# Kernel optimization log

Measured on AMD Instinct MI355X. Metric: run time of the kernel, lower is better.

## Reference

```python
import jax, jax.numpy as jnp
import numpy as np

B, S, H, NH, NKV, HD, E, I = 1, 2048, 1024, 16, 8, 64, 8, 2048
TOPK = 2
EPS = 1e-6
THETA = 1e6


def setup_inputs() -> dict:
    key = jax.random.key(0)
    ks = jax.random.split(key, 12)
    init = lambda k, shp: jax.random.normal(k, shp, jnp.float32) * 0.02
    hidden_states = jax.random.normal(ks[0], (B, S, H), jnp.float32)
    attention_mask = jnp.ones((B, S), jnp.float32)
    position_ids = jnp.broadcast_to(jnp.arange(S, dtype=jnp.int32), (B, S))
    inv_freq = 1.0 / (THETA ** (jnp.arange(0, HD, 2, dtype=jnp.float32) / HD))
    freqs = jnp.outer(jnp.arange(S, dtype=jnp.float32), inv_freq)  # [S, HD/2]
    emb = jnp.concatenate([freqs, freqs], axis=-1)                  # [S, HD]
    return dict(
        hidden_states=hidden_states,
        attention_mask=attention_mask,
        position_ids=position_ids,
        sin=jnp.sin(emb), cos=jnp.cos(emb),
        wq=init(ks[1], (H, NH * HD)),
        wk=init(ks[2], (H, NKV * HD)),
        wv=init(ks[3], (H, NKV * HD)),
        wo=init(ks[4], (NH * HD, H)),
        ln1=jnp.ones((H,), jnp.float32),
        ln2=jnp.ones((H,), jnp.float32),
        gate_w=init(ks[5], (H, E)),
        w1=init(ks[6], (E, H, I)),
        w3=init(ks[7], (E, H, I)),
        w2=init(ks[8], (E, I, H)),
    )


def _rms_norm(x, w):
    return x * jax.lax.rsqrt(jnp.mean(jnp.square(x), -1, keepdims=True) + EPS) * w


def _rotate_half(x):
    h = x.shape[-1] // 2
    return jnp.concatenate([-x[..., h:], x[..., :h]], axis=-1)


def reference(hidden_states, attention_mask, position_ids, sin, cos,
              wq, wk, wv, wo, ln1, ln2, gate_w, w1, w3, w2):
    x = hidden_states
    # ---- self-attention block ----
    h = _rms_norm(x, ln1)
    q = (h @ wq).reshape(B, S, NH, HD).transpose(0, 2, 1, 3)    # [B,NH,S,HD]
    k = (h @ wk).reshape(B, S, NKV, HD).transpose(0, 2, 1, 3)   # [B,NKV,S,HD]
    v = (h @ wv).reshape(B, S, NKV, HD).transpose(0, 2, 1, 3)
    sb = sin[position_ids][:, None]  # [B,1,S,HD]
    cb = cos[position_ids][:, None]
    q = q * cb + _rotate_half(q) * sb
    k = k * cb + _rotate_half(k) * sb
    rep = NH // NKV
    k = jnp.repeat(k, rep, axis=1)  # GQA repeat -> [B,NH,S,HD]
    v = jnp.repeat(v, rep, axis=1)
    causal = jnp.tril(jnp.ones((S, S), bool))
    mask = causal[None, None] & (attention_mask[:, None, None, :] > 0)
    bias = jnp.where(mask, 0.0, jnp.finfo(jnp.float32).min)
    scale = 1.0 / jnp.sqrt(jnp.float32(HD))
    scores = jnp.einsum('bhqd,bhkd->bhqk', q, k) * scale + bias
    attn = jax.nn.softmax(scores, axis=-1)
    o = jnp.einsum('bhqk,bhkd->bhqd', attn, v)
    o = o.transpose(0, 2, 1, 3).reshape(B, S, NH * HD) @ wo
    x = x + o
    # ---- sparse MoE block (top-2 of E experts, SiLU-gated MLP) ----
    t = _rms_norm(x, ln2).reshape(B * S, H)
    router_logits = t @ gate_w                         # [T,E]
    probs = jax.nn.softmax(router_logits, axis=-1)
    top_w, top_i = jax.lax.top_k(probs, TOPK)          # [T,2]
    top_w = top_w / jnp.sum(top_w, axis=-1, keepdims=True)
    full_w = jnp.sum(jax.nn.one_hot(top_i, E, dtype=t.dtype) * top_w[..., None], axis=1)  # [T,E]
    moe_out = jnp.zeros_like(t)
    for e in range(E):  # fixed small expert count
        ge = jax.nn.silu(t @ w1[e]) * (t @ w3[e])      # [T,I]
        moe_out = moe_out + full_w[:, e:e + 1] * (ge @ w2[e])
    x = x + moe_out.reshape(B, S, H)
    return x
```

## Files before the change

### kernel.cpp

```cpp
#include <hip/hip_runtime.h>

#define S 2048
#define H 1024
#define NH 16
#define NKV 8
#define HD 64
#define NE 8
#define ID 2048

typedef short bf16x8 __attribute__((ext_vector_type(8)));
typedef short bf16x4 __attribute__((ext_vector_type(4)));
typedef float f32x4 __attribute__((ext_vector_type(4)));

__device__ __forceinline__ unsigned short f2bf(float f) {
  unsigned u = __builtin_bit_cast(unsigned, f);
  u += 0x7FFFu + ((u >> 16) & 1u);
  return (unsigned short)(u >> 16);
}
__device__ __forceinline__ float bf2f(unsigned short h) {
  unsigned u = ((unsigned)h) << 16;
  return __builtin_bit_cast(float, u);
}
__device__ __forceinline__ unsigned cvtpk(float a, float b) {
  unsigned r;
  asm("v_cvt_pk_bf16_f32 %0, %1, %2" : "=v"(r) : "v"(a), "v"(b));
  return r;
}

typedef const __attribute__((address_space(1))) unsigned int gas_u32;
typedef __attribute__((address_space(3))) unsigned int las_u32;
__device__ __forceinline__ void gload16(const unsigned short* g, unsigned short* l) {
  __builtin_amdgcn_global_load_lds((gas_u32*)g, (las_u32*)l, 16, 0, 0);
}

template <bool LO>
__device__ __forceinline__ void tconv_tile128(const float* __restrict__ src,
                                              unsigned short* __restrict__ hi,
                                              unsigned short* __restrict__ lo, int K, int N,
                                              int nt, int kt, float (*tile)[65]) {
  int tid = threadIdx.x;
  int wv = tid >> 6, ln = tid & 63;
  const float* sb = src + (size_t)(kt * 128) * N + nt * 64 + ln;
#pragma unroll 8
  for (int rr = 0; rr < 32; rr++) {
    int r = rr * 4 + wv;
    tile[r][ln] = sb[(size_t)r * N];
  }
  __syncthreads();
  int seg = tid & 15;
  int rq = tid >> 4;
#pragma unroll
  for (int it = 0; it < 4; it++) {
    int row = it * 16 + rq;
    int cs = seg * 8;
    size_t dbase = (size_t)(nt * 64 + row) * K + kt * 128 + cs;
    unsigned short th[8], tl[8];
#pragma unroll
    for (int i = 0; i < 8; i++) {
      float vv = tile[cs + i][row];
      unsigned short h_ = f2bf(vv);
      th[i] = h_;
      if (LO) tl[i] = f2bf(vv - bf2f(h_));
    }
    *(bf16x8*)(hi + dbase) = *(bf16x8*)&th[0];
    if (LO) *(bf16x8*)(lo + dbase) = *(bf16x8*)&tl[0];
  }
}

__global__ __launch_bounds__(256) void prep_kernel(
    const float* __restrict__ x, const float* __restrict__ ln1,
    unsigned short* __restrict__ h_hi, unsigned short* __restrict__ h_lo,
    const float* __restrict__ wq, const float* __restrict__ wk, const float* __restrict__ wv,
    const float* __restrict__ wo, unsigned short* __restrict__ wqkvT_hi,
    unsigned short* __restrict__ wqkvT_lo, unsigned short* __restrict__ woT_hi,
    unsigned short* __restrict__ woT_lo) {
  __shared__ float tile[128][65];
  __shared__ float part[4];
  int u = blockIdx.x, grp = u / 19, slot = u % 19;
  int tid = threadIdx.x;
  if (slot < 16) {
    int row = grp * 16 + slot;
    const float* xr = x + (size_t)row * H;
    float v[4];
    float ss = 0.f;
#pragma unroll
    for (int i = 0; i < 4; i++) {
      v[i] = xr[tid + i * 256];
      ss += v[i] * v[i];
    }
#pragma unroll
    for (int off = 1; off < 64; off <<= 1) ss += __shfl_xor(ss, off);
    if ((tid & 63) == 0) part[tid >> 6] = ss;
    __syncthreads();
    float tot = part[0] + part[1] + part[2] + part[3];
    float r = rsqrtf(tot * (1.f / H) + 1e-6f);
#pragma unroll
    for (int i = 0; i < 4; i++) {
      int c = tid + i * 256;
      float vv = v[i] * r * ln1[c];
      size_t o = (size_t)row * H + c;
      unsigned short h_ = f2bf(vv);
      h_hi[o] = h_;
      h_lo[o] = f2bf(vv - bf2f(h_));
    }
  } else {
    int local = grp * 3 + (slot - 16);
    const float* src;
    unsigned short *hi, *lo;
    int N, l2;
    if (local < 128) {
      src = wq; hi = wqkvT_hi; lo = wqkvT_lo; N = 1024; l2 = local;
    } else if (local < 192) {
      src = wk; hi = wqkvT_hi + (size_t)1024 * 1024; lo = wqkvT_lo + (size_t)1024 * 1024; N = 512; l2 = local - 128;
    } else if (local < 256) {
      src = wv; hi = wqkvT_hi + (size_t)1536 * 1024; lo = wqkvT_lo + (size_t)1536 * 1024; N = 512; l2 = local - 192;
    } else {
      src = wo; hi = woT_hi; lo = woT_lo; N = 1024; l2 = local - 256;
    }
    int ntc = N >> 6;
    int nt = l2 % ntc, kt = l2 / ntc;
    tconv_tile128<true>(src, hi, lo, 1024, N, nt, kt, tile);
  }
}

__global__ __launch_bounds__(256) void rv_kernel(
    const float* __restrict__ qkv, const float* __restrict__ sinb,
    const float* __restrict__ cosb, const int* __restrict__ pos,
    unsigned short* __restrict__ qhi, unsigned short* __restrict__ qlo,
    unsigned short* __restrict__ khi, unsigned short* __restrict__ klo,
    unsigned short* __restrict__ vThi, unsigned short* __restrict__ vTlo) {
  __shared__ float tile[64][65];
  int u = blockIdx.x, grp = u / 25, slot = u % 25;
  int tid = threadIdx.x;
  if (slot == 0) {
    int st = grp & 31, hk = grp >> 5;
    int r = tid >> 2, seg = (tid & 3) * 16;
    const float* src = qkv + (size_t)(st * 64 + r) * 2048 + 1536 + hk * HD + seg;
#pragma unroll
    for (int i = 0; i < 16; i += 4) {
      float4 a = *(const float4*)(src + i);
      tile[r][seg + i] = a.x;
      tile[r][seg + i + 1] = a.y;
      tile[r][seg + i + 2] = a.z;
      tile[r][seg + i + 3] = a.w;
    }
    __syncthreads();
    int d = tid >> 2, ss = (tid & 3) * 16;
    unsigned short th[16], tl[16];
#pragma unroll
    for (int i = 0; i < 16; i++) {
      float vv = tile[ss + i][d];
      unsigned short h_ = f2bf(vv);
      th[i] = h_;
      tl[i] = f2bf(vv - bf2f(h_));
    }
    size_t dst = ((size_t)hk * HD + d) * S + st * 64 + ss;
    *(bf16x8*)(vThi + dst) = *(bf16x8*)&th[0];
    *(bf16x8*)(vThi + dst + 8) = *(bf16x8*)&th[8];
    *(bf16x8*)(vTlo + dst) = *(bf16x8*)&tl[0];
    *(bf16x8*)(vTlo + dst + 8) = *(bf16x8*)&tl[8];
  } else {
    int i = (grp * 24 + slot - 1) * 256 + tid;
    int d = i & 31;
    int s = (i >> 5) & 2047;
    int hh = i >> 16;
    int p = pos[s];
    float c0 = cosb[p * HD + d], c1 = cosb[p * HD + d + 32];
    float s0 = sinb[p * HD + d], s1 = sinb[p * HD + d + 32];
    const float* srcb = qkv + (size_t)s * 2048;
    if (hh < NH) {
      float x0 = srcb[hh * HD + d], x1 = srcb[hh * HD + d + 32];
      float r0 = (x0 * c0 - x1 * s0) * 0.125f;
      float r1 = (x1 * c1 + x0 * s1) * 0.125f;
      size_t o = ((size_t)hh * S + s) * HD + d;
      unsigned short h0 = f2bf(r0), h1 = f2bf(r1);
      qhi[o] = h0;
      qlo[o] = f2bf(r0 - bf2f(h0));
      qhi[o + 32] = h1;
      qlo[o + 32] = f2bf(r1 - bf2f(h1));
    } else {
      int hk = hh - NH;
      float x0 = srcb[1024 + hk * HD + d], x1 = srcb[1024 + hk * HD + d + 32];
      float r0 = x0 * c0 - x1 * s0;
      float r1 = x1 * c1 + x0 * s1;
      size_t o = ((size_t)hk * S + s) * HD + d;
      unsigned short h0 = f2bf(r0), h1 = f2bf(r1);
      khi[o] = h0;
      klo[o] = f2bf(r0 - bf2f(h0));
      khi[o + 32] = h1;
      klo[o + 32] = f2bf(r1 - bf2f(h1));
    }
  }
}

__global__ __launch_bounds__(256, 4) void gemm1_w13_kernel(
    const unsigned short* __restrict__ oh, const unsigned short* __restrict__ ol,
    const unsigned short* __restrict__ woh, const unsigned short* __restrict__ wol,
    float* __restrict__ x2, float* __restrict__ out, const float* __restrict__ resid,
    const float* __restrict__ w1, const float* __restrict__ w3,
    unsigned short* __restrict__ w1T, unsigned short* __restrict__ w3T) {
  __shared__ __align__(16) char smem[33280];
  int u = blockIdx.x, grp = u / 9, slot = u % 9;
  int tid = threadIdx.x;
  if (slot != 0) {
    int t = grp * 8 + slot - 1;
    int b = t >> 8, rem = t & 255, kt = rem >> 5, nt = rem & 31;
    const float* src = (b < 8) ? w1 + (size_t)b * 1024 * 2048 : w3 + (size_t)(b - 8) * 1024 * 2048;
    unsigned short* hi = (b < 8) ? w1T + (size_t)b * 2048 * 1024 : w3T + (size_t)(b - 8) * 2048 * 1024;
    tconv_tile128<false>(src, hi, nullptr, 1024, 2048, nt, kt, (float(*)[65])smem);
    return;
  }
  int g = grp;
  int bx = g & 15, by = g >> 4;
  unsigned short* tAh = (unsigned short*)smem;
  unsigned short* tAl = tAh + 4096;
  unsigned short* tBh = tAl + 4096;
  unsigned short* tBl = tBh + 4096;
  int n0 = bx * 64, m0 = by * 64;
  int w = tid >> 6, lane = tid & 63;
  int lr = lane & 15, gq = lane >> 4;
  int rloc = lane >> 3, slotg = (lane & 7) ^ rloc;
  int wm = w >> 1, wn = w & 1;
  unsigned aOff[2], bOff[2];
#pragma unroll
  for (int cc = 0; cc < 2; cc++) {
    int rr = (w * 2 + cc) * 8 + rloc;
    aOff[cc] = (unsigned)((m0 + rr) * 1024 + slotg * 8);
    bOff[cc] = (unsigned)((n0 + rr) * 1024 + slotg * 8);
  }
  f32x4 acc[2][2];
#pragma unroll
  for (int i = 0; i < 2; i++)
#pragma unroll
    for (int j = 0; j < 2; j++) acc[i][j] = f32x4{0.f, 0.f, 0.f, 0.f};
  for (int k0 = 0; k0 < 1024; k0 += 64) {
    __syncthreads();
#pragma unroll
    for (int cc = 0; cc < 2; cc++) {
      int cb = (w * 2 + cc) * 512;
      gload16(oh + aOff[cc] + k0, &tAh[cb]);
      gload16(ol + aOff[cc] + k0, &tAl[cb]);
      gload16(woh + bOff[cc] + k0, &tBh[cb]);
      gload16(wol + bOff[cc] + k0, &tBl[cb]);
    }
    __syncthreads();
    bf16x8 fah[2][2], fal[2][2];
#pragma unroll
    for (int i = 0; i < 2; i++) {
      int ar = wm * 32 + i * 16 + lr;
#pragma unroll
      for (int kk = 0; kk < 2; kk++) {
        int off = ar * 64 + (((kk * 4 + gq) ^ (ar & 7)) * 8);
        fah[i][kk] = *(const bf16x8*)&tAh[off];
        fal[i][kk] = *(const bf16x8*)&tAl[off];
      }
    }
#pragma unroll
    for (int j = 0; j < 2; j++) {
      int br = wn * 32 + j * 16 + lr;
      bf16x8 fbh[2], fbl[2];
#pragma unroll
      for (int kk = 0; kk < 2; kk++) {
        int off = br * 64 + (((kk * 4 + gq) ^ (br & 7)) * 8);
        fbh[kk] = *(const bf16x8*)&tBh[off];
        fbl[kk] = *(const bf16x8*)&tBl[off];
      }
#pragma unroll
      for (int i = 0; i < 2; i++) {
#pragma unroll
        for (int kk = 0; kk < 2; kk++) {
          acc[i][j] = __builtin_amdgcn_mfma_f32_16x16x32_bf16(fah[i][kk], fbh[kk], acc[i][j], 0, 0, 0);
          acc[i][j] = __builtin_amdgcn_mfma_f32_16x16x32_bf16(fah[i][kk], fbl[kk], acc[i][j], 0, 0, 0);
          acc[i][j] = __builtin_amdgcn_mfma_f32_16x16x32_bf16(fal[i][kk], fbh[kk], acc[i][j], 0, 0, 0);
        }
      }
    }
  }
#pragma unroll
  for (int i = 0; i < 2; i++)
#pragma unroll
    for (int j = 0; j < 2; j++)
#pragma unroll
      for (int r = 0; r < 4; r++) {
        int grow = wm * 32 + i * 16 + gq * 4 + r;
        int gcol = n0 + wn * 32 + j * 16 + lr;
        float o = acc[i][j][r] + resid[(size_t)(m0 + grow) * 1024 + gcol];
        x2[(size_t)(m0 + grow) * 1024 + gcol] = o;
        out[(size_t)(m0 + grow) * 1024 + gcol] = o;
      }
}

__global__ __launch_bounds__(256) void rmsnorm_router_kernel(
    const float* __restrict__ x, const float* __restrict__ wgt,
    const float* __restrict__ gw, unsigned short* __restrict__ ohi,
    int* __restrict__ selE, float* __restrict__ selW) {
  int row = blockIdx.x;
  const float* xr = x + (size_t)row * H;
  int tid = threadIdx.x;
  float v[4];
  float ss = 0.f;
#pragma unroll
  for (int i = 0; i < 4; i++) {
    v[i] = xr[tid + i * 256];
    ss += v[i] * v[i];
  }
#pragma unroll
  for (int off = 1; off < 64; off <<= 1) ss += __shfl_xor(ss, off);
  __shared__ float part[4];
  __shared__ float red[4][NE];
  if ((tid & 63) == 0) part[tid >> 6] = ss;
  __syncthreads();
  float tot = part[0] + part[1] + part[2] + part[3];
  float r = rsqrtf(tot * (1.f / H) + 1e-6f);
  float acc[NE];
#pragma unroll
  for (int e = 0; e < NE; e++) acc[e] = 0.f;
#pragma unroll
  for (int i = 0; i < 4; i++) {
    int c = tid + i * 256;
    float vv = v[i] * r * wgt[c];
    ohi[(size_t)row * H + c] = f2bf(vv);
    const float4* gp = (const float4*)(gw + (size_t)c * NE);
    float4 g0 = gp[0], g1 = gp[1];
    acc[0] += vv * g0.x;
    acc[1] += vv * g0.y;
    acc[2] += vv * g0.z;
    acc[3] += vv * g0.w;
    acc[4] += vv * g1.x;
    acc[5] += vv * g1.y;
    acc[6] += vv * g1.z;
    acc[7] += vv * g1.w;
  }
#pragma unroll
  for (int off = 1; off < 64; off <<= 1) {
#pragma unroll
    for (int e = 0; e < NE; e++) acc[e] += __shfl_xor(acc[e], off);
  }
  if ((tid & 63) == 0) {
#pragma unroll
    for (int e = 0; e < NE; e++) red[tid >> 6][e] = acc[e];
  }
  __syncthreads();
  if (tid == 0) {
    float lg[NE];
#pragma unroll
    for (int e = 0; e < NE; e++) lg[e] = red[0][e] + red[1][e] + red[2][e] + red[3][e];
    int e1 = 0;
#pragma unroll
    for (int e = 1; e < NE; e++)
      if (lg[e] > lg[e1]) e1 = e;
    int e2 = -1;
#pragma unroll
    for (int e = 0; e < NE; e++)
      if (e != e1 && (e2 < 0 || lg[e] > lg[e2])) e2 = e;
    float w1v = 1.f / (1.f + __expf(lg[e2] - lg[e1]));
    selE[row] = e1 | (e2 << 8);
    selW[row * 2] = w1v;
    selW[row * 2 + 1] = 1.f - w1v;
  }
}

__global__ __launch_bounds__(256) void assign_kernel(const int* __restrict__ selE,
                                                     int* __restrict__ cnt,
                                                     int* __restrict__ offs,
                                                     int* __restrict__ tmap,
                                                     int* __restrict__ idxb,
                                                     int* __restrict__ tokslot) {
  int tid = threadIdx.x;
  __shared__ int sc[256][NE];
  int pack[8];
  int hist[NE];
#pragma unroll
  for (int e = 0; e < NE; e++) hist[e] = 0;
#pragma unroll
  for (int i = 0; i < 8; i++) {
    pack[i] = selE[tid * 8 + i];
    hist[pack[i] & 255]++;
    hist[(pack[i] >> 8) & 255]++;
  }
#pragma unroll
  for (int e = 0; e < NE; e++) sc[tid][e] = hist[e];
  __syncthreads();
  for (int off = 1; off < 256; off <<= 1) {
    int add[NE];
    bool has = tid >= off;
    if (has) {
#pragma unroll
      for (int e = 0; e < NE; e++) add[e] = sc[tid - off][e];
    }
    __syncthreads();
    if (has) {
#pragma unroll
      for (int e = 0; e < NE; e++) sc[tid][e] += add[e];
    }
    __syncthreads();
  }
  int offsL[NE];
  {
    int a = 0;
#pragma unroll
    for (int e = 0; e < NE; e++) {
      offsL[e] = a;
      a += sc[255][e];
    }
  }
  if (tid == 0) {
    int t = 0;
    for (int e = 0; e < NE; e++) {
      int totE = sc[255][e];
      offs[e] = offsL[e];
      cnt[e] = totE;
      int nt = (totE + 127) >> 7;
      for (int i = 0; i < nt; i++) tmap[t++] = (e << 16) | i;
    }
    offs[NE] = offsL[NE - 1] + sc[255][NE - 1];
    tmap[63] = t;
  }
  int run[NE];
#pragma unroll
  for (int e = 0; e < NE; e++) run[e] = sc[tid][e] - hist[e];
#pragma unroll
  for (int i = 0; i < 8; i++) {
    int tok = tid * 8 + i;
    int e1 = pack[i] & 255, e2 = (pack[i] >> 8) & 255;
    int p1 = run[e1]++;
    idxb[e1 * S + p1] = tok;
    int p2 = run[e2]++;
    idxb[e2 * S + p2] = tok;
    tokslot[tok * 2] = offsL[e1] + p1;
    tokslot[tok * 2 + 1] = offsL[e2] + p2;
  }
}

__global__ __launch_bounds__(256) void moe_gather_kernel(const float* __restrict__ moeP,
                                                         const int* __restrict__ tokslot,
                                                         const float* __restrict__ selW,
                                                         float* __restrict__ out) {
  int tok = blockIdx.x;
  int c = threadIdx.x * 4;
  int s0 = tokslot[tok * 2], s1 = tokslot[tok * 2 + 1];
  float w0 = selW[tok * 2], w1 = selW[tok * 2 + 1];
  const float* P0 = moeP;
  const float* P1 = moeP + (size_t)4096 * 1024;
  float4 a0 = *(const float4*)(P0 + (size_t)s0 * 1024 + c);
  float4 b0 = *(const float4*)(P1 + (size_t)s0 * 1024 + c);
  float4 a1 = *(const float4*)(P0 + (size_t)s1 * 1024 + c);
  float4 b1 = *(const float4*)(P1 + (size_t)s1 * 1024 + c);
  float* op = out + (size_t)tok * 1024 + c;
  float4 o = *(float4*)op;
  o.x += w0 * (a0.x + b0.x) + w1 * (a1.x + b1.x);
  o.y += w0 * (a0.y + b0.y) + w1 * (a1.y + b1.y);
  o.z += w0 * (a0.z + b0.z) + w1 * (a1.z + b1.z);
  o.w += w0 * (a0.w + b0.w) + w1 * (a1.w + b1.w);
  *(float4*)op = o;
}

__global__ __launch_bounds__(256, 4) void tconv_w2_kernel(const float* __restrict__ w2,
                                                          unsigned short* __restrict__ w2T) {
  __shared__ float tile[128][65];
  int b = blockIdx.z;
  tconv_tile128<false>(w2 + (size_t)b * 2048 * 1024, w2T + (size_t)b * 1024 * 2048, nullptr, 2048,
                       1024, blockIdx.x, blockIdx.y, tile);
}

template <int MODE>
__global__ __launch_bounds__(256, 4) void gemm_kernel(
    const unsigned short* __restrict__ Ah, const unsigned short* __restrict__ Al,
    const unsigned short* __restrict__ Bh, const unsigned short* __restrict__ Bl,
    float* __restrict__ C, unsigned short* __restrict__ Gout,
    const int* __restrict__ idx, const int* __restrict__ cnt, const int* __restrict__ offs,
    const int* __restrict__ tmap, int N, int K) {
  constexpr int BM = (MODE <= 1) ? 64 : 128;
  constexpr int NI = BM / 32;
  int n0 = blockIdx.x * 64, m0, e = 0;
  int ce = 0, gbase = 0;
  if (MODE >= 2) {
    int ntiles = tmap[63];
    if ((int)blockIdx.y >= ntiles) return;
    int packed = tmap[blockIdx.y];
    e = packed >> 16;
    m0 = (packed & 0xffff) * 128;
    ce = cnt[e];
    gbase = offs[e];
  } else {
    m0 = blockIdx.y * BM;
  }
  const unsigned short* bhp = Bh;
  const unsigned short* blp = Bl;
  if (MODE == 2) {
    bhp += (size_t)e * 2048 * 1024;
    blp += (size_t)e * 2048 * 1024;
  }
  if (MODE == 3) bhp += (size_t)e * 1024 * 2048;

  __shared__ __align__(16) unsigned short tAh[BM * 64];
  __shared__ __align__(16) unsigned short tAl[MODE <= 1 ? BM * 64 : 8];
  __shared__ __align__(16) unsigned short tBh[64 * 64];
  __shared__ __align__(16) unsigned short tBl[MODE <= 2 ? 64 * 64 : 8];

  int tid = threadIdx.x, w = tid >> 6, lane = tid & 63;
  int lr = lane & 15, g = lane >> 4;
  int rloc = lane >> 3, slotg = (lane & 7) ^ rloc;
  int wm = w >> 1, wn = w & 1;

  unsigned aOff[NI], bOff[2];
#pragma unroll
  for (int cc = 0; cc < NI; cc++) {
    int rr = (w * NI + cc) * 8 + rloc;
    if (MODE == 2) {
      int gr = m0 + rr;
      if (gr > ce - 1) gr = ce - 1;
      int tok = idx[e * S + gr];
      aOff[cc] = (unsigned)(tok * K + slotg * 8);
    } else if (MODE == 3) {
      int gr = gbase + m0 + rr;
      if (gr > 4095) gr = 4095;
      aOff[cc] = (unsigned)(gr * K + slotg * 8);
    } else {
      aOff[cc] = (unsigned)((m0 + rr) * K + slotg * 8);
    }
  }
#pragma unroll
  for (int cc = 0; cc < 2; cc++) {
    int rr = (w * 2 + cc) * 8 + rloc;
    bOff[cc] = (unsigned)((n0 + rr) * K + slotg * 8);
  }

  f32x4 acc[NI][2], acc2[NI][2];
#pragma unroll
  for (int i = 0; i < NI; i++)
#pragma unroll
    for (int j = 0; j < 2; j++) {
      acc[i][j] = f32x4{0.f, 0.f, 0.f, 0.f};
      if (MODE == 2) acc2[i][j] = f32x4{0.f, 0.f, 0.f, 0.f};
    }

  int kbeg = 0, kend = K;
  if (MODE == 3) {
    kbeg = (int)blockIdx.z * (K >> 1);
    kend = kbeg + (K >> 1);
  }
  for (int k0 = kbeg; k0 < kend; k0 += 64) {
    __syncthreads();
#pragma unroll
    for (int cc = 0; cc < NI; cc++) {
      int cb = (w * NI + cc) * 512;
      gload16(Ah + aOff[cc] + k0, &tAh[cb]);
      if (MODE <= 1) gload16(Al + aOff[cc] + k0, &tAl[cb]);
    }
#pragma unroll
    for (int cc = 0; cc < 2; cc++) {
      int cb = (w * 2 + cc) * 512;
      gload16(bhp + bOff[cc] + k0, &tBh[cb]);
      if (MODE <= 2) gload16(blp + bOff[cc] + k0, &tBl[cb]);
    }
    __syncthreads();
    bf16x8 fah[NI][2], fal[NI][2];
#pragma unroll
    for (int i = 0; i < NI; i++) {
      int ar = wm * (BM / 2) + i * 16 + lr;
#pragma unroll
      for (int kk = 0; kk < 2; kk++) {
        int off = ar * 64 + (((kk * 4 + g) ^ (ar & 7)) * 8);
        fah[i][kk] = *(const bf16x8*)&tAh[off];
        if (MODE <= 1) fal[i][kk] = *(const bf16x8*)&tAl[off];
      }
    }
#pragma unroll
    for (int j = 0; j < 2; j++) {
      int br = wn * 32 + j * 16 + lr;
      bf16x8 fbh[2], fbl[2];
#pragma unroll
      for (int kk = 0; kk < 2; kk++) {
        int off = br * 64 + (((kk * 4 + g) ^ (br & 7)) * 8);
        fbh[kk] = *(const bf16x8*)&tBh[off];
        if (MODE <= 2) fbl[kk] = *(const bf16x8*)&tBl[off];
      }
#pragma unroll
      for (int i = 0; i < NI; i++) {
#pragma unroll
        for (int kk = 0; kk < 2; kk++) {
          acc[i][j] = __builtin_amdgcn_mfma_f32_16x16x32_bf16(fah[i][kk], fbh[kk], acc[i][j], 0, 0, 0);
          if (MODE <= 1) {
            acc[i][j] = __builtin_amdgcn_mfma_f32_16x16x32_bf16(fah[i][kk], fbl[kk], acc[i][j], 0, 0, 0);
            acc[i][j] = __builtin_amdgcn_mfma_f32_16x16x32_bf16(fal[i][kk], fbh[kk], acc[i][j], 0, 0, 0);
          }
          if (MODE == 2)
            acc2[i][j] = __builtin_amdgcn_mfma_f32_16x16x32_bf16(fah[i][kk], fbl[kk], acc2[i][j], 0, 0, 0);
        }
      }
    }
  }
#pragma unroll
  for (int i = 0; i < NI; i++)
#pragma unroll
    for (int j = 0; j < 2; j++)
#pragma unroll
      for (int r = 0; r < 4; r++) {
        int grow = wm * (BM / 2) + i * 16 + g * 4 + r;
        int gcol = n0 + wn * 32 + j * 16 + lr;
        float v = acc[i][j][r];
        if (MODE == 0) {
          C[(size_t)(m0 + grow) * N + gcol] = v;
        } else if (MODE == 2) {
          if (m0 + grow < ce) {
            float g3 = acc2[i][j][r];
            float sg = v / (1.f + __expf(-v));
            Gout[(size_t)(gbase + m0 + grow) * 2048 + gcol] = f2bf(sg * g3);
          }
        } else if (MODE == 3) {
          if (m0 + grow < ce) {
            C[(size_t)blockIdx.z * 4096 * 1024 + (size_t)(gbase + m0 + grow) * 1024 + gcol] = v;
          }
        }
      }
}

#define FSWZ(row, byteoff) ((byteoff) ^ (((row) & 7) << 4))

__global__ __launch_bounds__(256, 4) void flash_kernel(
    const unsigned short* __restrict__ qhi, const unsigned short* __restrict__ qlo,
    const unsigned short* __restrict__ khip, const unsigned short* __restrict__ klop,
    const unsigned short* __restrict__ vthip, const unsigned short* __restrict__ vtlop,
    const float* __restrict__ amask, float* __restrict__ po, float* __restrict__ pm,
    float* __restrict__ pl) {
  int u = blockIdx.x;
  int r_ = u >> 8, base = u & 255;
  int qt = (base + r_ * 8) & 31;
  int head = ((base >> 5) & 7) | ((r_ & 1) << 3);
  int z = r_ >> 1;
  int tid = threadIdx.x;
  int w = tid >> 6, lane = tid & 63;
  int lr = lane & 15, g = lane >> 4;
  int rloc = lane >> 3, slotg = (lane & 7) ^ rloc;

  __shared__ __align__(16) unsigned short Khi[64 * 64];
  __shared__ __align__(16) unsigned short Klo[64 * 64];
  __shared__ __align__(16) unsigned short Vhi[64 * 64];
  __shared__ __align__(16) unsigned short Vlo[64 * 64];
  __shared__ __align__(16) unsigned short Pbuf[4][16 * 64];

  int qrow = qt * 64 + w * 16 + lr;
  bf16x8 qh[2], ql[2];
  {
    const unsigned short* qb = qhi + ((size_t)head * S + qrow) * HD;
    const unsigned short* qb2 = qlo + ((size_t)head * S + qrow) * HD;
    qh[0] = *(const bf16x8*)(qb + g * 8);
    qh[1] = *(const bf16x8*)(qb + 32 + g * 8);
    ql[0] = *(const bf16x8*)(qb2 + g * 8);
    ql[1] = *(const bf16x8*)(qb2 + 32 + g * 8);
  }

  f32x4 oacc[4];
#pragma unroll
  for (int dg = 0; dg < 4; dg++) oacc[dg] = f32x4{0.f, 0.f, 0.f, 0.f};
  float m = -1e30f, l = 0.f;

  const unsigned short* kbh = khip + (size_t)(head >> 1) * S * HD;
  const unsigned short* kbl = klop + (size_t)(head >> 1) * S * HD;
  const unsigned short* vbh = vthip + (size_t)(head >> 1) * HD * S;
  const unsigned short* vbl = vtlop + (size_t)(head >> 1) * HD * S;
  char* pbase = (char*)Pbuf[w];

  int nblk = qt + 1;
  int b0 = (z * nblk) >> 1, b1 = ((z + 1) * nblk) >> 1;

  for (int kb = b0; kb < b1; kb++) {
    int kv0 = kb * 64;
    __syncthreads();
#pragma unroll
    for (int cc = 0; cc < 2; cc++) {
      int c = w * 2 + cc;
      int r = c * 8 + rloc;
      gload16(kbh + (size_t)(kv0 + r) * HD + slotg * 8, &Khi[c * 512]);
      gload16(kbl + (size_t)(kv0 + r) * HD + slotg * 8, &Klo[c * 512]);
      gload16(vbh + (size_t)r * S + kv0 + slotg * 8, &Vhi[c * 512]);
      gload16(vbl + (size_t)r * S + kv0 + slotg * 8, &Vlo[c * 512]);
    }
    unsigned long long vm = __ballot(amask[kv0 + lane] > 0.f);
    __syncthreads();

    f32x4 sacc[4];
#pragma unroll
    for (int c = 0; c < 4; c++) sacc[c] = f32x4{0.f, 0.f, 0.f, 0.f};
#pragma unroll
    for (int c = 0; c < 4; c++) {
#pragma unroll
      for (int kc = 0; kc < 2; kc++) {
        int row = c * 16 + lr;
        int bo = FSWZ(row, row * 128 + kc * 64 + g * 16);
        bf16x8 khf = *(const bf16x8*)((char*)Khi + bo);
        bf16x8 klf = *(const bf16x8*)((char*)Klo + bo);
        sacc[c] = __builtin_amdgcn_mfma_f32_16x16x32_bf16(khf, qh[kc], sacc[c], 0, 0, 0);
        sacc[c] = __builtin_amdgcn_mfma_f32_16x16x32_bf16(khf, ql[kc], sacc[c], 0, 0, 0);
        sacc[c] = __builtin_amdgcn_mfma_f32_16x16x32_bf16(klf, qh[kc], sacc[c], 0, 0, 0);
      }
    }
    int qloc = w * 16 + lr;
    bool diag = (kb == qt);
    bool fullvis = (vm == ~0ull) && !diag;
    float tm = -1e30f;
    if (fullvis) {
#pragma unroll
      for (int c = 0; c < 4; c++)
#pragma unroll
        for (int r = 0; r < 4; r++) tm = fmaxf(tm, sacc[c][r]);
    } else {
#pragma unroll
      for (int c = 0; c < 4; c++) {
#pragma unroll
        for (int r = 0; r < 4; r++) {
          int kvloc = c * 16 + 4 * g + r;
          bool vis = ((vm >> kvloc) & 1ull) && (!diag || kvloc <= qloc);
          float sv = vis ? sacc[c][r] : -1e30f;
          sacc[c][r] = sv;
          tm = fmaxf(tm, sv);
        }
      }
    }
    tm = fmaxf(tm, __shfl_xor(tm, 16));
    tm = fmaxf(tm, __shfl_xor(tm, 32));
    bool skip = __all(tm - m <= 8.f);
    float newm = skip ? m : fmaxf(m, tm);
    float rs = 0.f;
#pragma unroll
    for (int c = 0; c < 4; c++) {
#pragma unroll
      for (int r = 0; r < 4; r++) {
        float p = __expf(sacc[c][r] - newm);
        sacc[c][r] = p;
        rs += p;
      }
    }
    rs += __shfl_xor(rs, 16);
    rs += __shfl_xor(rs, 32);
    if (!skip) {
      float alpha = __expf(m - newm);
      m = newm;
      l = l * alpha + rs;
#pragma unroll
      for (int dg = 0; dg < 4; dg++) {
#pragma unroll
        for (int r = 0; r < 4; r++) oacc[dg][r] *= alpha;
      }
    } else {
      l += rs;
    }
    unsigned hw[4][2];
#pragma unroll
    for (int c = 0; c < 4; c++) {
      hw[c][0] = cvtpk(sacc[c][0], sacc[c][1]);
      hw[c][1] = cvtpk(sacc[c][2], sacc[c][3]);
      uint2 hv = {hw[c][0], hw[c][1]};
      *(uint2*)(pbase + FSWZ(lr, lr * 128 + (c * 16 + 4 * g) * 2)) = hv;
    }
    bf16x8 pbh[2], pbl[2];
#pragma unroll
    for (int kc = 0; kc < 2; kc++)
      pbh[kc] = *(const bf16x8*)(pbase + FSWZ(lr, lr * 128 + kc * 64 + g * 16));
#pragma unroll
    for (int c = 0; c < 4; c++) {
      float h0 = __builtin_bit_cast(float, hw[c][0] << 16);
      float h1 = __builtin_bit_cast(float, hw[c][0] & 0xffff0000u);
      float h2 = __builtin_bit_cast(float, hw[c][1] << 16);
      float h3 = __builtin_bit_cast(float, hw[c][1] & 0xffff0000u);
      uint2 lv = {cvtpk(sacc[c][0] - h0, sacc[c][1] - h1),
                  cvtpk(sacc[c][2] - h2, sacc[c][3] - h3)};
      *(uint2*)(pbase + FSWZ(lr, lr * 128 + (c * 16 + 4 * g) * 2)) = lv;
    }
#pragma unroll
    for (int kc = 0; kc < 2; kc++)
      pbl[kc] = *(const bf16x8*)(pbase + FSWZ(lr, lr * 128 + kc * 64 + g * 16));
#pragma unroll
    for (int dg = 0; dg < 4; dg++) {
#pragma unroll
      for (int kc = 0; kc < 2; kc++) {
        int row = dg * 16 + lr;
        int bo = FSWZ(row, row * 128 + kc * 64 + g * 16);
        bf16x8 vhf = *(const bf16x8*)((char*)Vhi + bo);
        bf16x8 vlf = *(const bf16x8*)((char*)Vlo + bo);
        oacc[dg] = __builtin_amdgcn_mfma_f32_16x16x32_bf16(vhf, pbh[kc], oacc[dg], 0, 0, 0);
        oacc[dg] = __builtin_amdgcn_mfma_f32_16x16x32_bf16(vhf, pbl[kc], oacc[dg], 0, 0, 0);
        oacc[dg] = __builtin_amdgcn_mfma_f32_16x16x32_bf16(vlf, pbh[kc], oacc[dg], 0, 0, 0);
      }
    }
  }

  size_t pb = (size_t)(qt * 16 + head) * 2 + z;
  int row = w * 16 + lr;
  if (g == 0) {
    pm[pb * 64 + row] = m;
    pl[pb * 64 + row] = l;
  }
  float* pob = po + pb * 4096 + (size_t)row * 64;
#pragma unroll
  for (int dg = 0; dg < 4; dg++) {
    float4 v4 = {oacc[dg][0], oacc[dg][1], oacc[dg][2], oacc[dg][3]};
    *(float4*)(pob + dg * 16 + 4 * g) = v4;
  }
}

__global__ __launch_bounds__(256) void combine_kernel(const float* __restrict__ po,
                                                      const float* __restrict__ pm,
                                                      const float* __restrict__ pl,
                                                      unsigned short* __restrict__ ohi,
                                                      unsigned short* __restrict__ olo) {
  int qt = blockIdx.x, head = blockIdx.y;
  int r = threadIdx.x >> 2, dg = (threadIdx.x & 3) * 16;
  size_t base = (size_t)(qt * 16 + head) * 2;
  float m0v = pm[base * 64 + r], m1v = pm[(base + 1) * 64 + r];
  float l0 = pl[base * 64 + r], l1 = pl[(base + 1) * 64 + r];
  float M = fmaxf(m0v, m1v);
  float w0 = __expf(m0v - M), w1 = __expf(m1v - M);
  float inv = 1.f / (w0 * l0 + w1 * l1);
  const float* p0 = po + base * 4096 + (size_t)r * 64 + dg;
  const float* p1 = po + (base + 1) * 4096 + (size_t)r * 64 + dg;
  unsigned short th[16], tl[16];
#pragma unroll
  for (int i = 0; i < 16; i += 4) {
    float4 a = *(const float4*)(p0 + i);
    float4 b = *(const float4*)(p1 + i);
    float vv[4] = {(w0 * a.x + w1 * b.x) * inv, (w0 * a.y + w1 * b.y) * inv,
                   (w0 * a.z + w1 * b.z) * inv, (w0 * a.w + w1 * b.w) * inv};
#pragma unroll
    for (int j = 0; j < 4; j++) {
      unsigned short h_ = f2bf(vv[j]);
      th[i + j] = h_;
      tl[i + j] = f2bf(vv[j] - bf2f(h_));
    }
  }
  size_t ob = (size_t)(qt * 64 + r) * 1024 + head * 64 + dg;
  *(bf16x8*)(ohi + ob) = *(bf16x8*)&th[0];
  *(bf16x8*)(ohi + ob + 8) = *(bf16x8*)&th[8];
  *(bf16x8*)(olo + ob) = *(bf16x8*)&tl[0];
  *(bf16x8*)(olo + ob + 8) = *(bf16x8*)&tl[8];
}

extern "C" void kernel_launch(void* const* d_in, const int* in_sizes, int n_in,
                              void* d_out, int out_size, void* d_ws, size_t ws_size,
                              hipStream_t stream) {
  const float* x = (const float*)d_in[0];
  const float* amask = (const float*)d_in[1];
  const int* pos = (const int*)d_in[2];
  const float* sinb = (const float*)d_in[3];
  const float* cosb = (const float*)d_in[4];
  const float* wq = (const float*)d_in[5];
  const float* wk = (const float*)d_in[6];
  const float* wv = (const float*)d_in[7];
  const float* wo = (const float*)d_in[8];
  const float* ln1 = (const float*)d_in[9];
  const float* ln2 = (const float*)d_in[10];
  const float* gw = (const float*)d_in[11];
  const float* w1 = (const float*)d_in[12];
  const float* w3 = (const float*)d_in[13];
  const float* w2 = (const float*)d_in[14];
  float* out = (float*)d_out;

  char* ws = (char*)d_ws;
  const size_t MB = 1024 * 1024;
  float* x2 = (float*)(ws + 0 * MB);
  unsigned short* t_bf = (unsigned short*)(ws + 8 * MB);
  int* cnt = (int*)(ws + 12 * MB);
  int* offs = cnt + 16;
  int* tmap = cnt + 32;
  int* idxb = cnt + 128;
  int* selE = idxb + 16384;
  int* tokslot = selE + 2048;
  float* selW = (float*)(tokslot + 4096);
  unsigned short* o_hi = (unsigned short*)(ws + 13 * MB);
  unsigned short* o_lo = (unsigned short*)(ws + 17 * MB);
  unsigned short* G = (unsigned short*)(ws + 13 * MB);
  float* qkv = (float*)(ws + 13 * MB);
  unsigned short* w1T = (unsigned short*)(ws + 29 * MB);
  unsigned short* w3T = (unsigned short*)(ws + 61 * MB);
  unsigned short* w2T = (unsigned short*)(ws + 29 * MB);
  float* moeP = (float*)(ws + 61 * MB);
  float* po = (float*)(ws + 29 * MB);
  float* pm = (float*)(ws + 45 * MB);
  float* pl = (float*)(ws + 46 * MB);
  unsigned short* wqkvT_hi = (unsigned short*)(ws + 47 * MB);
  unsigned short* wqkvT_lo = (unsigned short*)(ws + 51 * MB);
  unsigned short* h_hi = (unsigned short*)(ws + 55 * MB);
  unsigned short* h_lo = (unsigned short*)(ws + 59 * MB);
  unsigned short* q_hi = (unsigned short*)(ws + 63 * MB);
  unsigned short* q_lo = (unsigned short*)(ws + 67 * MB);
  unsigned short* k_hi = (unsigned short*)(ws + 71 * MB);
  unsigned short* k_lo = (unsigned short*)(ws + 73 * MB);
  unsigned short* vT_hi = (unsigned short*)(ws + 75 * MB);
  unsigned short* vT_lo = (unsigned short*)(ws + 77 * MB);
  unsigned short* woT_hi = (unsigned short*)(ws + 93 * MB);
  unsigned short* woT_lo = (unsigned short*)(ws + 95 * MB);

  prep_kernel<<<2432, 256, 0, stream>>>(x, ln1, h_hi, h_lo, wq, wk, wv, wo, wqkvT_hi, wqkvT_lo,
                                        woT_hi, woT_lo);
  gemm_kernel<0><<<dim3(32, 32, 1), 256, 0, stream>>>(h_hi, h_lo, wqkvT_hi, wqkvT_lo, qkv, nullptr,
                                                      nullptr, nullptr, nullptr, nullptr, 2048,
                                                      1024);
  rv_kernel<<<6400, 256, 0, stream>>>(qkv, sinb, cosb, pos, q_hi, q_lo, k_hi, k_lo, vT_hi, vT_lo);
  flash_kernel<<<dim3(1024, 1, 1), 256, 0, stream>>>(q_hi, q_lo, k_hi, k_lo, vT_hi, vT_lo, amask,
                                                     po, pm, pl);
  combine_kernel<<<dim3(32, 16), 256, 0, stream>>>(po, pm, pl, o_hi, o_lo);
  gemm1_w13_kernel<<<4608, 256, 0, stream>>>(o_hi, o_lo, woT_hi, woT_lo, x2, out, x, w1, w3, w1T,
                                             w3T);
  rmsnorm_router_kernel<<<S, 256, 0, stream>>>(x2, ln2, gw, t_bf, selE, selW);
  assign_kernel<<<1, 256, 0, stream>>>(selE, cnt, offs, tmap, idxb, tokslot);
  gemm_kernel<2><<<dim3(32, 40, 1), 256, 0, stream>>>(t_bf, nullptr, w1T, w3T, nullptr, G, idxb,
                                                      cnt, offs, tmap, 2048, 1024);
  tconv_w2_kernel<<<dim3(16, 16, 8), 256, 0, stream>>>(w2, w2T);
  gemm_kernel<3><<<dim3(16, 40, 2), 256, 0, stream>>>(G, nullptr, w2T, nullptr, moeP, nullptr,
                                                      idxb, cnt, offs, tmap, 1024, 2048);
  moe_gather_kernel<<<S, 256, 0, stream>>>(moeP, tokslot, selW, out);
}
```

Baseline: 281.3 us.

## Fuse w2 transpose-convert into grouped w1/w3 MoE GEMM launch

Merges the expert w1/w3 gated GEMM and the w2 transpose/bf16 conversion into one kernel launch. Blocks are interleaved in groups of 13: 5 GEMM tiles and 8 transpose tiles, so the memory-bound conversion can run alongside the compute-bound GEMM. w2T moves to its own workspace region so it no longer aliases w1T. This removes a launch boundary and idle tail, at the cost of the shared-memory footprint being sized for the larger of the two roles.

```diff
diff --git a/kernel.cpp b/kernel.cpp
--- a/kernel.cpp
+++ b/kernel.cpp
@@ -290,6 +290,123 @@
       }
 }
 
+__global__ __launch_bounds__(256, 4) void gemm2_w2_kernel(
+    const unsigned short* __restrict__ Ah, const unsigned short* __restrict__ w1T,
+    const unsigned short* __restrict__ w3T, unsigned short* __restrict__ Gout,
+    const int* __restrict__ idx, const int* __restrict__ cnt, const int* __restrict__ offs,
+    const int* __restrict__ tmap, const float* __restrict__ w2,
+    unsigned short* __restrict__ w2T) {
+  __shared__ __align__(16) char smem[33280];
+  int u = blockIdx.x, grp = u / 13, slot = u % 13;
+  int tid = threadIdx.x;
+  if (slot >= 5) {
+    int t = grp * 8 + slot - 5;
+    int b = t >> 8, rem = t & 255, kt = rem >> 4, nt = rem & 15;
+    tconv_tile128<false>(w2 + (size_t)b * 2048 * 1024, w2T + (size_t)b * 1024 * 2048, nullptr,
+                         2048, 1024, nt, kt, (float(*)[65])smem);
+    return;
+  }
+  int g = grp * 5 + slot;
+  int bx = g & 31, ty = g >> 5;
+  int ntiles = tmap[63];
+  if (ty >= ntiles) return;
+  int packed = tmap[ty];
+  int e = packed >> 16;
+  int m0 = (packed & 0xffff) * 128;
+  int ce = cnt[e];
+  int gbase = offs[e];
+  const unsigned short* bhp = w1T + (size_t)e * 2048 * 1024;
+  const unsigned short* blp = w3T + (size_t)e * 2048 * 1024;
+  unsigned short* tAh = (unsigned short*)smem;
+  unsigned short* tBh = tAh + 8192;
+  unsigned short* tBl = tBh + 4096;
+  int n0 = bx * 64;
+  int w = tid >> 6, lane = tid & 63;
+  int lr = lane & 15, gq = lane >> 4;
+  int rloc = lane >> 3, slotg = (lane & 7) ^ rloc;
+  int wm = w >> 1, wn = w & 1;
+  unsigned aOff[4], bOff[2];
+#pragma unroll
+  for (int cc = 0; cc < 4; cc++) {
+    int rr = (w * 4 + cc) * 8 + rloc;
+    int gr = m0 + rr;
+    if (gr > ce - 1) gr = ce - 1;
+    int tok = idx[e * S + gr];
+    aOff[cc] = (unsigned)(tok * 1024 + slotg * 8);
+  }
+#pragma unroll
+  for (int cc = 0; cc < 2; cc++) {
+    int rr = (w * 2 + cc) * 8 + rloc;
+    bOff[cc] = (unsigned)((n0 + rr) * 1024 + slotg * 8);
+  }
+  f32x4 acc[4][2], acc2[4][2];
+#pragma unroll
+  for (int i = 0; i < 4; i++)
+#pragma unroll
+    for (int j = 0; j < 2; j++) {
+      acc[i][j] = f32x4{0.f, 0.f, 0.f, 0.f};
+      acc2[i][j] = f32x4{0.f, 0.f, 0.f, 0.f};
+    }
+  for (int k0 = 0; k0 < 1024; k0 += 64) {
+    __syncthreads();
+#pragma unroll
+    for (int cc = 0; cc < 4; cc++) {
+      gload16(Ah + aOff[cc] + k0, &tAh[(w * 4 + cc) * 512]);
+    }
+#pragma unroll
+    for (int cc = 0; cc < 2; cc++) {
+      int cb = (w * 2 + cc) * 512;
+      gload16(bhp + bOff[cc] + k0, &tBh[cb]);
+      gload16(blp + bOff[cc] + k0, &tBl[cb]);
+    }
+    __syncthreads();
+    bf16x8 fah[4][2];
+#pragma unroll
+    for (int i = 0; i < 4; i++) {
+      int ar = wm * 64 + i * 16 + lr;
+#pragma unroll
+      for (int kk = 0; kk < 2; kk++) {
+        int off = ar * 64 + (((kk * 4 + gq) ^ (ar & 7)) * 8);
+        fah[i][kk] = *(const bf16x8*)&tAh[off];
+      }
+    }
+#pragma unroll
+    for (int j = 0; j < 2; j++) {
+      int br = wn * 32 + j * 16 + lr;
+      bf16x8 fbh[2], fbl[2];
+#pragma unroll
+      for (int kk = 0; kk < 2; kk++) {
+        int off = br * 64 + (((kk * 4 + gq) ^ (br & 7)) * 8);
+        fbh[kk] = *(const bf16x8*)&tBh[off];
+        fbl[kk] = *(const bf16x8*)&tBl[off];
+      }
+#pragma unroll
+      for (int i = 0; i < 4; i++) {
+#pragma unroll
+        for (int kk = 0; kk < 2; kk++) {
+          acc[i][j] = __builtin_amdgcn_mfma_f32_16x16x32_bf16(fah[i][kk], fbh[kk], acc[i][j], 0, 0, 0);
+          acc2[i][j] = __builtin_amdgcn_mfma_f32_16x16x32_bf16(fah[i][kk], fbl[kk], acc2[i][j], 0, 0, 0);
+        }
+      }
+    }
+  }
+#pragma unroll
+  for (int i = 0; i < 4; i++)
+#pragma unroll
+    for (int j = 0; j < 2; j++)
+#pragma unroll
+      for (int r = 0; r < 4; r++) {
+        int grow = wm * 64 + i * 16 + gq * 4 + r;
+        int gcol = n0 + wn * 32 + j * 16 + lr;
+        if (m0 + grow < ce) {
+          float v = acc[i][j][r];
+          float g3 = acc2[i][j][r];
+          float sg = v / (1.f + __expf(-v));
+          Gout[(size_t)(gbase + m0 + grow) * 2048 + gcol] = f2bf(sg * g3);
+        }
+      }
+}
+
 __global__ __launch_bounds__(256) void rmsnorm_router_kernel(
     const float* __restrict__ x, const float* __restrict__ wgt,
     const float* __restrict__ gw, unsigned short* __restrict__ ohi,
@@ -455,14 +572,6 @@
   *(float4*)op = o;
 }
 
-__global__ __launch_bounds__(256, 4) void tconv_w2_kernel(const float* __restrict__ w2,
-                                                          unsigned short* __restrict__ w2T) {
-  __shared__ float tile[128][65];
-  int b = blockIdx.z;
-  tconv_tile128<false>(w2 + (size_t)b * 2048 * 1024, w2T + (size_t)b * 1024 * 2048, nullptr, 2048,
-                       1024, blockIdx.x, blockIdx.y, tile);
-}
-
 template <int MODE>
 __global__ __launch_bounds__(256, 4) void gemm_kernel(
     const unsigned short* __restrict__ Ah, const unsigned short* __restrict__ Al,
@@ -487,10 +596,6 @@
   }
   const unsigned short* bhp = Bh;
   const unsigned short* blp = Bl;
-  if (MODE == 2) {
-    bhp += (size_t)e * 2048 * 1024;
-    blp += (size_t)e * 2048 * 1024;
-  }
   if (MODE == 3) bhp += (size_t)e * 1024 * 2048;
 
   __shared__ __align__(16) unsigned short tAh[BM * 64];
@@ -507,12 +612,7 @@
 #pragma unroll
   for (int cc = 0; cc < NI; cc++) {
     int rr = (w * NI + cc) * 8 + rloc;
-    if (MODE == 2) {
-      int gr = m0 + rr;
-      if (gr > ce - 1) gr = ce - 1;
-      int tok = idx[e * S + gr];
-      aOff[cc] = (unsigned)(tok * K + slotg * 8);
-    } else if (MODE == 3) {
+    if (MODE == 3) {
       int gr = gbase + m0 + rr;
       if (gr > 4095) gr = 4095;
       aOff[cc] = (unsigned)(gr * K + slotg * 8);
@@ -526,14 +626,11 @@
     bOff[cc] = (unsigned)((n0 + rr) * K + slotg * 8);
   }
 
-  f32x4 acc[NI][2], acc2[NI][2];
+  f32x4 acc[NI][2];
 #pragma unroll
   for (int i = 0; i < NI; i++)
 #pragma unroll
-    for (int j = 0; j < 2; j++) {
-      acc[i][j] = f32x4{0.f, 0.f, 0.f, 0.f};
-      if (MODE == 2) acc2[i][j] = f32x4{0.f, 0.f, 0.f, 0.f};
-    }
+    for (int j = 0; j < 2; j++) acc[i][j] = f32x4{0.f, 0.f, 0.f, 0.f};
 
   int kbeg = 0, kend = K;
   if (MODE == 3) {
@@ -585,8 +682,6 @@
             acc[i][j] = __builtin_amdgcn_mfma_f32_16x16x32_bf16(fah[i][kk], fbl[kk], acc[i][j], 0, 0, 0);
             acc[i][j] = __builtin_amdgcn_mfma_f32_16x16x32_bf16(fal[i][kk], fbh[kk], acc[i][j], 0, 0, 0);
           }
-          if (MODE == 2)
-            acc2[i][j] = __builtin_amdgcn_mfma_f32_16x16x32_bf16(fah[i][kk], fbl[kk], acc2[i][j], 0, 0, 0);
         }
       }
     }
@@ -602,12 +697,6 @@
         float v = acc[i][j][r];
         if (MODE == 0) {
           C[(size_t)(m0 + grow) * N + gcol] = v;
-        } else if (MODE == 2) {
-          if (m0 + grow < ce) {
-            float g3 = acc2[i][j][r];
-            float sg = v / (1.f + __expf(-v));
-            Gout[(size_t)(gbase + m0 + grow) * 2048 + gcol] = f2bf(sg * g3);
-          }
         } else if (MODE == 3) {
           if (m0 + grow < ce) {
             C[(size_t)blockIdx.z * 4096 * 1024 + (size_t)(gbase + m0 + grow) * 1024 + gcol] = v;
@@ -873,7 +962,6 @@
   float* qkv = (float*)(ws + 13 * MB);
   unsigned short* w1T = (unsigned short*)(ws + 29 * MB);
   unsigned short* w3T = (unsigned short*)(ws + 61 * MB);
-  unsigned short* w2T = (unsigned short*)(ws + 29 * MB);
   float* moeP = (float*)(ws + 61 * MB);
   float* po = (float*)(ws + 29 * MB);
   float* pm = (float*)(ws + 45 * MB);
@@ -890,6 +978,7 @@
   unsigned short* vT_lo = (unsigned short*)(ws + 77 * MB);
   unsigned short* woT_hi = (unsigned short*)(ws + 93 * MB);
   unsigned short* woT_lo = (unsigned short*)(ws + 95 * MB);
+  unsigned short* w2T = (unsigned short*)(ws + 97 * MB);
 
   prep_kernel<<<2432, 256, 0, stream>>>(x, ln1, h_hi, h_lo, wq, wk, wv, wo, wqkvT_hi, wqkvT_lo,
                                         woT_hi, woT_lo);
@@ -904,9 +993,7 @@
                                              w3T);
   rmsnorm_router_kernel<<<S, 256, 0, stream>>>(x2, ln2, gw, t_bf, selE, selW);
   assign_kernel<<<1, 256, 0, stream>>>(selE, cnt, offs, tmap, idxb, tokslot);
-  gemm_kernel<2><<<dim3(32, 40, 1), 256, 0, stream>>>(t_bf, nullptr, w1T, w3T, nullptr, G, idxb,
-                                                      cnt, offs, tmap, 2048, 1024);
-  tconv_w2_kernel<<<dim3(16, 16, 8), 256, 0, stream>>>(w2, w2T);
+  gemm2_w2_kernel<<<3328, 256, 0, stream>>>(t_bf, w1T, w3T, G, idxb, cnt, offs, tmap, w2, w2T);
   gemm_kernel<3><<<dim3(16, 40, 2), 256, 0, stream>>>(G, nullptr, w2T, nullptr, moeP, nullptr,
                                                       idxb, cnt, offs, tmap, 1024, 2048);
   moe_gather_kernel<<<S, 256, 0, stream>>>(moeP, tokslot, selW, out);
```

Result: faster. 272.6 us (-3.1%).
